# Kernel optimization log

Hardware: AMD Instinct MI355X
Metric: run time of the kernel (lower is better)

Reference implementation:

```python
import jax, jax.numpy as jnp
import numpy as np

ROI_SIZE = 7
MAX_BIN_H = 8   # max adaptive-maxpool bin height for crop H <= 37
MAX_BIN_W = 9   # max adaptive-maxpool bin width  for crop W <= 50
SCALE = 0.0625  # 1/16 feature stride


def setup_inputs() -> dict:
    key = jax.random.key(0)
    ks = jax.random.split(key, 12)
    B, C, h, w = 1, 512, 37, 50          # conv5 feature map of a 600x800 image
    N = 512                               # number of ROIs (proposals)
    n_class = 21
    d_in, d_fc = C * ROI_SIZE * ROI_SIZE, 4096
    x = jax.random.normal(ks[0], (B, C, h, w), dtype=jnp.float32)
    # rois in image coordinates (x1, y1, x2, y2), image is 800x600
    x1 = jax.random.uniform(ks[1], (N,), minval=0.0, maxval=700.0)
    y1 = jax.random.uniform(ks[2], (N,), minval=0.0, maxval=500.0)
    bw = jax.random.uniform(ks[3], (N,), minval=16.0, maxval=400.0)
    bh = jax.random.uniform(ks[4], (N,), minval=16.0, maxval=300.0)
    rois = jnp.stack([x1, y1, jnp.minimum(x1 + bw, 799.0), jnp.minimum(y1 + bh, 599.0)], axis=1).astype(jnp.float32)
    roi_index = jnp.zeros((N,), dtype=jnp.int32)  # single image in batch
    W1 = jax.random.normal(ks[5], (d_in, d_fc), dtype=jnp.float32) * 0.01
    b1 = jnp.zeros((d_fc,), dtype=jnp.float32)
    W2 = jax.random.normal(ks[6], (d_fc, d_fc), dtype=jnp.float32) * 0.01
    b2 = jnp.zeros((d_fc,), dtype=jnp.float32)
    Wp = jax.random.normal(ks[7], (d_fc, n_class * 4), dtype=jnp.float32) * 0.001
    bp = jax.random.normal(ks[8], (n_class * 4,), dtype=jnp.float32) * 0.001
    Ws = jax.random.normal(ks[9], (d_fc, n_class), dtype=jnp.float32) * 0.01
    bs = jax.random.normal(ks[10], (n_class,), dtype=jnp.float32) * 0.01
    return dict(x=x, rois=rois, roi_index=roi_index, W1=W1, b1=b1, W2=W2, b2=b2, Wp=Wp, bp=bp, Ws=Ws, bs=bs)


def _roi_pool(x, rois, roi_index):
    """Faithful port of roi_pooling(): per-ROI crop + AdaptiveMaxPool2d(7)."""
    B, C, h, w = x.shape
    S = ROI_SIZE
    coords = jnp.round(rois * SCALE)  # round-half-even, like torch.round
    cx1 = jnp.clip(coords[:, 0], 0, w).astype(jnp.int32)
    cy1 = jnp.clip(coords[:, 1], 0, h).astype(jnp.int32)
    cx2 = jnp.clip(coords[:, 2], 0, w).astype(jnp.int32)
    cy2 = jnp.clip(coords[:, 3], 0, h).astype(jnp.int32)
    bidx = roi_index.astype(jnp.int32)
    roi_stack = jnp.stack([bidx, cx1, cy1, cx2, cy2], axis=1)  # [N,5]

    def pool_one(carry, roi):
        bi, x1i, y1i, x2i, y2i = roi[0], roi[1], roi[2], roi[3], roi[4]
        valid = (x1i < x2i) & (y1i < y2i)
        # torch slicing roi[2]:roi[4]+1 silently truncates at the tensor edge
        x2e = jnp.minimum(x2i, w - 1)
        y2e = jnp.minimum(y2i, h - 1)
        Hc = y2e - y1i + 1
        Wc = x2e - x1i + 1
        i = jnp.arange(S)
        # adaptive max pool bins: [floor(i*H/S), ceil((i+1)*H/S))
        rs = y1i + (i * Hc) // S
        re = y1i + ((i + 1) * Hc + S - 1) // S
        cs = x1i + (i * Wc) // S
        ce = x1i + ((i + 1) * Wc + S - 1) // S
        rows = rs[:, None] + jnp.arange(MAX_BIN_H)          # [S, MBH]
        rmask = rows < re[:, None]
        rows = jnp.clip(rows, 0, h - 1)
        cols = cs[:, None] + jnp.arange(MAX_BIN_W)          # [S, MBW]
        cmask = cols < ce[:, None]
        cols = jnp.clip(cols, 0, w - 1)
        feat = x[bi]                                         # [C, h, w]
        g = feat[:, rows[:, None, :, None], cols[None, :, None, :]]  # [C,S,S,MBH,MBW]
        mask = rmask[:, None, :, None] & cmask[None, :, None, :]     # [S,S,MBH,MBW]
        pooled = jnp.where(mask, g, -jnp.inf).max(axis=(-2, -1))    # [C,S,S]
        pooled = jnp.where(valid, pooled, jnp.zeros_like(pooled))
        return carry, pooled

    _, out = jax.lax.scan(pool_one, None, roi_stack)  # [N, C, S, S]
    return out


def reference(x, rois, roi_index, W1, b1, W2, b2, Wp, bp, Ws, bs):
    pooled = _roi_pool(x, rois, roi_index)            # [N, 512, 7, 7]
    flat = pooled.reshape(pooled.shape[0], -1)        # [N, 25088]
    fc6 = jax.nn.relu(flat @ W1 + b1)                 # [N, 4096]
    fc7 = jax.nn.relu(fc6 @ W2 + b2)                  # [N, 4096]
    roi_class_params = fc7 @ Wp + bp                  # [N, n_class*4]
    roi_scores = fc7 @ Ws + bs                        # [N, n_class]
    return (roi_class_params, roi_scores)
```

## Files before the change

kernel.cpp:

```cpp
#include <hip/hip_runtime.h>
#include <hip/hip_bf16.h>

using f32x4  = float          __attribute__((ext_vector_type(4)));
using bf16x8 = __bf16         __attribute__((ext_vector_type(8)));
using u16x8  = unsigned short __attribute__((ext_vector_type(8)));

#define C_CH 512
#define H_IN 37
#define W_IN 50
#define NPOS 1850
#define NROI 512
#define DIN  25088
#define DFC  4096
#define NPAR 84
#define NCLS 21
#define KS1  4
#define KS2  4
#define KSH  8

#define PB_X  232
#define PB_WH 2048
#define PB_TOT (PB_X + PB_WH)

__device__ __forceinline__ unsigned pack_bf16x2(float a, float b) {
    __hip_bfloat162 h;
    h.x = __float2bfloat16(a);
    h.y = __float2bfloat16(b);
    return *reinterpret_cast<unsigned*>(&h);
}

__device__ __forceinline__ void gload_lds16(const void* src, void* dst) {
    __builtin_amdgcn_global_load_lds(
        (const __attribute__((address_space(1))) void*)src,
        (__attribute__((address_space(3))) void*)dst, 16, 0, 0);
}

__global__ __launch_bounds__(256) void prep_kernel(
        const float* __restrict__ x, float* __restrict__ xt,
        const float* __restrict__ Wp, const float* __restrict__ Ws,
        float* __restrict__ Whp) {
    __shared__ float tile[64][65];
    int b = blockIdx.x;
    int t = threadIdx.x;
    if (b < PB_X) {
        int p0 = (b % 29) * 64;
        int c0 = (b / 29) * 64;
        int tc = t & 63, tr = t >> 6;
#pragma unroll
        for (int i = 0; i < 16; ++i) {
            int r = tr + i * 4;
            int p = p0 + tc;
            float v = 0.f;
            if (p < NPOS) v = x[(size_t)(c0 + r) * NPOS + p];
            tile[r][tc] = v;
        }
        __syncthreads();
#pragma unroll
        for (int i = 0; i < 16; ++i) {
            int rw = tr + i * 4;
            int p = p0 + rw;
            if (p < NPOS) xt[(size_t)p * C_CH + c0 + tc] = tile[tc][rw];
        }
    } else {
        int idx = (b - PB_X) * 256 + t;
        int k = idx >> 7, c = idx & 127;
        float v = 0.f;
        if (c < NPAR) v = Wp[(size_t)k * NPAR + c];
        else if (c < NPAR + NCLS) v = Ws[(size_t)k * NCLS + (c - NPAR)];
        Whp[idx] = v;
    }
}

__global__ __launch_bounds__(256) void roi_pool_kernel(
        const float* __restrict__ xt, const float* __restrict__ rois,
        __hip_bfloat16* __restrict__ pooled) {
    int n = blockIdx.x;
    int t = threadIdx.x;
    float4 rv = reinterpret_cast<const float4*>(rois)[n];
    int x1 = (int)fminf(fmaxf(rintf(rv.x * 0.0625f), 0.f), (float)W_IN);
    int y1 = (int)fminf(fmaxf(rintf(rv.y * 0.0625f), 0.f), (float)H_IN);
    int x2 = (int)fminf(fmaxf(rintf(rv.z * 0.0625f), 0.f), (float)W_IN);
    int y2 = (int)fminf(fmaxf(rintf(rv.w * 0.0625f), 0.f), (float)H_IN);
    bool valid = (x1 < x2) && (y1 < y2);
    unsigned* outp = reinterpret_cast<unsigned*>(pooled) + (size_t)n * (DIN / 2);
    if (!valid) {
        for (int b = 0; b < 49; ++b) outp[b * 256 + t] = 0u;
        return;
    }
    int x2e = min(x2, W_IN - 1), y2e = min(y2, H_IN - 1);
    int Hc = y2e - y1 + 1, Wc = x2e - x1 + 1;
    const float2* base = reinterpret_cast<const float2*>(xt);
    for (int i = 0; i < 7; ++i) {
        int rs = y1 + (i * Hc) / 7;
        int re = y1 + ((i + 1) * Hc + 6) / 7;
        for (int j = 0; j < 7; ++j) {
            int cs = x1 + (j * Wc) / 7;
            int ce = x1 + ((j + 1) * Wc + 6) / 7;
            float m0 = -__builtin_inff(), m1 = -__builtin_inff();
            for (int r = rs; r < re; ++r) {
                const float2* rowp = base + (size_t)r * (W_IN * C_CH / 2) + t;
                for (int c = cs; c < ce; ++c) {
                    float2 v = rowp[c * (C_CH / 2)];
                    m0 = fmaxf(m0, v.x);
                    m1 = fmaxf(m1, v.y);
                }
            }
            outp[(i * 7 + j) * 256 + t] = pack_bf16x2(m0, m1);
        }
    }
}

__global__ __launch_bounds__(256) void gemm_f32b_kernel(
        const __hip_bfloat16* __restrict__ A,
        const float* __restrict__ Bf,
        float* __restrict__ Cp,
        int N, int lda, int ldbn, int kChunk, int nMT, int nNT, int Mtot,
        int perm) {
    __shared__ __align__(16) char lA[3 * 16384];
    __shared__ __align__(16) char lB[2 * 16384];

    int q = gridDim.x >> 3;
    int bid = (blockIdx.x & 7) * q + (blockIdx.x >> 3);
    int mt = bid % nMT;
    int nt = (bid / nMT) % nNT;
    int ks = bid / (nMT * nNT);
    int m0 = mt * 128, n0 = nt * 128;
    int k0 = ks * kChunk;
    int t = threadIdx.x;
    int lane = t & 63, wid = t >> 6;

    const char* srcA[4]; int offA[4];
#pragma unroll
    for (int i = 0; i < 4; ++i) {
        int chunk = i * 4 + wid;
        int p = chunk * 1024 + lane * 16;
        int row = p >> 7;
        int swz = ((row ^ (row >> 3)) & 7) << 4;
        srcA[i] = (const char*)A + ((size_t)(m0 + row) * lda + k0) * 2
                  + ((p & 127) ^ swz);
        offA[i] = chunk * 1024;
    }
    auto stageA = [&](char* slot) {
#pragma unroll
        for (int i = 0; i < 4; ++i) {
            gload_lds16(srcA[i], slot + offA[i]);
            srcA[i] += 128;
        }
    };

    int n4 = (t & 31) * 4;
    int k8 = (t >> 5) * 8;
    int rstr = perm ? 49 : 1;
    const float* pB = Bf + n0 + n4;
    int koff[8];
#pragma unroll
    for (int p = 0; p < 8; ++p) koff[p] = (k8 + p) * rstr * ldbn;
    int woff[4];
#pragma unroll
    for (int j = 0; j < 4; ++j) {
        int row = n4 + j;
        int swz = ((row ^ (row >> 3)) & 7) << 4;
        woff[j] = row * 128 + ((k8 * 2) ^ swz);
    }
    auto loadB = [&](int kt, f32x4 (&v)[8]) {
        int kb = k0 + (kt << 6);
        int rb = perm ? ((kb & 511) * 49 + (kb >> 9)) : kb;
        int rbo = rb * ldbn;
#pragma unroll
        for (int p = 0; p < 8; ++p)
            v[p] = *reinterpret_cast<const f32x4*>(pB + (size_t)(rbo + koff[p]));
    };
    auto cvtB = [&](f32x4 (&v)[8], char* bW) {
#pragma unroll
        for (int j = 0; j < 4; ++j) {
            uint4 w;
            w.x = pack_bf16x2(v[0][j], v[1][j]);
            w.y = pack_bf16x2(v[2][j], v[3][j]);
            w.z = pack_bf16x2(v[4][j], v[5][j]);
            w.w = pack_bf16x2(v[6][j], v[7][j]);
            *reinterpret_cast<uint4*>(bW + woff[j]) = w;
        }
    };

    int wm = wid >> 1, wn = wid & 1;
    int kb0 = (lane >> 4) << 4;
    int roA[4], roB[4], sA[4], sB[4];
#pragma unroll
    for (int f = 0; f < 4; ++f) {
        int ra = wm * 64 + f * 16 + (lane & 15);
        int rb = wn * 64 + f * 16 + (lane & 15);
        roA[f] = ra * 128; sA[f] = ((ra ^ (ra >> 3)) & 7) << 4;
        roB[f] = rb * 128; sB[f] = ((rb ^ (rb >> 3)) & 7) << 4;
    }

    f32x4 acc[4][4] = {};
    auto mfmaHalf = [&](const char* bA, const char* bB, int ksub) {
        int kk = kb0 | (ksub << 6);
        bf16x8 af[4], bfr[4];
#pragma unroll
        for (int f = 0; f < 4; ++f)
            af[f] = *reinterpret_cast<const bf16x8*>(bA + roA[f] + (kk ^ sA[f]));
#pragma unroll
        for (int f = 0; f < 4; ++f)
            bfr[f] = *reinterpret_cast<const bf16x8*>(bB + roB[f] + (kk ^ sB[f]));
#pragma unroll
        for (int mf = 0; mf < 4; ++mf)
#pragma unroll
            for (int nf = 0; nf < 4; ++nf)
                acc[mf][nf] = __builtin_amdgcn_mfma_f32_16x16x32_bf16(
                    af[mf], bfr[nf], acc[mf][nf], 0, 0, 0);
    };

    int nkt = kChunk >> 6;

    f32x4 vP[8], vQ[8];
    auto body = [&](int tt, char* aR, char* aS,
                    f32x4 (&vC)[8], char* bR, char* bW) {
        mfmaHalf(aR, bR, 0);
        if (tt + 1 < nkt) cvtB(vC, bW);
        mfmaHalf(aR, bR, 1);
        if (tt + 2 < nkt) stageA(aS);
        if (tt + 3 < nkt) {
            loadB(tt + 3, vC);
            asm volatile("s_waitcnt vmcnt(12) lgkmcnt(0)\ns_barrier" ::: "memory");
        } else {
            asm volatile("s_waitcnt vmcnt(0) lgkmcnt(0)\ns_barrier" ::: "memory");
        }
    };

    stageA(lA);
    stageA(lA + 16384);
    loadB(0, vP);
    loadB(1, vQ);
    cvtB(vP, lB);
    loadB(2, vP);
    asm volatile("s_waitcnt vmcnt(12) lgkmcnt(0)\ns_barrier" ::: "memory");

    char* s0 = lA;  char* s1 = lA + 16384;  char* s2 = lA + 32768;
    char* b0 = lB;  char* b1 = lB + 16384;
    for (int kt = 0; kt < nkt; kt += 6) {
        body(kt + 0, s0, s2, vQ, b0, b1);
        if (kt + 1 < nkt) body(kt + 1, s1, s0, vP, b1, b0);
        if (kt + 2 < nkt) body(kt + 2, s2, s1, vQ, b0, b1);
        if (kt + 3 < nkt) body(kt + 3, s0, s2, vP, b1, b0);
        if (kt + 4 < nkt) body(kt + 4, s1, s0, vQ, b0, b1);
        if (kt + 5 < nkt) body(kt + 5, s2, s1, vP, b1, b0);
    }

    float* outp = Cp + (size_t)ks * Mtot * N;
    int rbase = m0 + wm * 64;
    int cbase = n0 + wn * 64 + (lane & 15);
    int rl = (lane >> 4) * 4;
#pragma unroll
    for (int mf = 0; mf < 4; ++mf)
#pragma unroll
        for (int nf = 0; nf < 4; ++nf)
#pragma unroll
            for (int r = 0; r < 4; ++r)
                outp[(size_t)(rbase + mf * 16 + rl + r) * N + cbase + nf * 16] =
                    acc[mf][nf][r];
}

__global__ __launch_bounds__(256) void reduce_bias_relu_kernel(
        const float* __restrict__ P, const float* __restrict__ bias,
        __hip_bfloat16* __restrict__ out, int MN, int N, int KS) {
    int idx = blockIdx.x * blockDim.x + threadIdx.x;
    int e0 = idx * 4;
    if (e0 >= MN) return;
    f32x4 s = *reinterpret_cast<const f32x4*>(P + e0);
    for (int k = 1; k < KS; ++k)
        s += *reinterpret_cast<const f32x4*>(P + (size_t)k * MN + e0);
    f32x4 b = *reinterpret_cast<const f32x4*>(bias + (e0 & (N - 1)));
    s += b;
    uint2 pk;
    pk.x = pack_bf16x2(fmaxf(s[0], 0.f), fmaxf(s[1], 0.f));
    pk.y = pack_bf16x2(fmaxf(s[2], 0.f), fmaxf(s[3], 0.f));
    *reinterpret_cast<uint2*>(reinterpret_cast<char*>(out) + (size_t)e0 * 2) = pk;
}

__global__ __launch_bounds__(128) void head_reduce_kernel(
        const float* __restrict__ P, const float* __restrict__ bp,
        const float* __restrict__ bs, float* __restrict__ out, int KS) {
    int n = blockIdx.x, c = threadIdx.x;
    float s = 0.f;
    for (int ks = 0; ks < KS; ++ks)
        s += P[(size_t)ks * NROI * 128 + (size_t)n * 128 + c];
    if (c < NPAR)
        out[(size_t)n * NPAR + c] = s + bp[c];
    else if (c < NPAR + NCLS)
        out[(size_t)NROI * NPAR + (size_t)n * NCLS + (c - NPAR)] = s + bs[c - NPAR];
}

extern "C" void kernel_launch(void* const* d_in, const int* in_sizes, int n_in,
                              void* d_out, int out_size, void* d_ws, size_t ws_size,
                              hipStream_t stream) {
    const float* x    = (const float*)d_in[0];
    const float* rois = (const float*)d_in[1];
    const float* W1 = (const float*)d_in[3];
    const float* b1 = (const float*)d_in[4];
    const float* W2 = (const float*)d_in[5];
    const float* b2 = (const float*)d_in[6];
    const float* Wp = (const float*)d_in[7];
    const float* bp = (const float*)d_in[8];
    const float* Ws = (const float*)d_in[9];
    const float* bs = (const float*)d_in[10];
    float* out = (float*)d_out;

    const size_t MB = 1ull << 20;
    char* ws = (char*)d_ws;
    float*          xt     = (float*)(ws + 0);
    __hip_bfloat16* pooled = (__hip_bfloat16*)(ws + 4   * MB);
    float*          Whp    = (float*)(ws + 30  * MB);
    float*          part   = (float*)(ws + 34  * MB);
    __hip_bfloat16* fc6    = (__hip_bfloat16*)(ws + 104 * MB);
    __hip_bfloat16* fc7    = (__hip_bfloat16*)(ws + 109 * MB);

    prep_kernel<<<PB_TOT, 256, 0, stream>>>(x, xt, Wp, Ws, Whp);
    roi_pool_kernel<<<NROI, 256, 0, stream>>>(xt, rois, pooled);

    gemm_f32b_kernel<<<4 * 32 * KS1, 256, 0, stream>>>(
        pooled, W1, part, DFC, DIN, DFC, DIN / KS1, 4, 32, NROI, 1);
    reduce_bias_relu_kernel<<<2048, 256, 0, stream>>>(part, b1, fc6,
                                                      NROI * DFC, DFC, KS1);

    gemm_f32b_kernel<<<4 * 32 * KS2, 256, 0, stream>>>(
        fc6, W2, part, DFC, DFC, DFC, DFC / KS2, 4, 32, NROI, 0);
    reduce_bias_relu_kernel<<<2048, 256, 0, stream>>>(part, b2, fc7,
                                                      NROI * DFC, DFC, KS2);

    gemm_f32b_kernel<<<4 * KSH, 256, 0, stream>>>(fc7, Whp, part,
                                                  128, DFC, 128, DFC / KSH,
                                                  4, 1, NROI, 0);
    head_reduce_kernel<<<NROI, 128, 0, stream>>>(part, bp, bs, out, KSH);
}
```

Before: 391.8 us.

## Shrink GEMM LDS ring and double split-K to raise occupancy

```diff
diff --git a/kernel.cpp b/kernel.cpp
--- a/kernel.cpp
+++ b/kernel.cpp
@@ -14,9 +14,9 @@
 #define DFC  4096
 #define NPAR 84
 #define NCLS 21
-#define KS1  4
-#define KS2  4
-#define KSH  8
+#define KS1  8
+#define KS2  8
+#define KSH  16
 
 #define PB_X  232
 #define PB_WH 2048
@@ -110,14 +110,15 @@
     }
 }
 
-__global__ __launch_bounds__(256) void gemm_f32b_kernel(
+__global__ __launch_bounds__(256, 3) void gemm_f32b_kernel(
         const __hip_bfloat16* __restrict__ A,
         const float* __restrict__ Bf,
         float* __restrict__ Cp,
         int N, int lda, int ldbn, int kChunk, int nMT, int nNT, int Mtot,
         int perm) {
-    __shared__ __align__(16) char lA[3 * 16384];
-    __shared__ __align__(16) char lB[2 * 16384];
+    __shared__ __align__(16) char lA0[16384];
+    __shared__ __align__(16) char lA1[16384];
+    __shared__ __align__(16) char lB[16384];
 
     int q = gridDim.x >> 3;
     int bid = (blockIdx.x & 7) * q + (blockIdx.x >> 3);
@@ -162,7 +163,8 @@
         int swz = ((row ^ (row >> 3)) & 7) << 4;
         woff[j] = row * 128 + ((k8 * 2) ^ swz);
     }
-    auto loadB = [&](int kt, f32x4 (&v)[8]) {
+    f32x4 v[8];
+    auto loadB = [&](int kt) {
         int kb = k0 + (kt << 6);
         int rb = perm ? ((kb & 511) * 49 + (kb >> 9)) : kb;
         int rbo = rb * ldbn;
@@ -170,7 +172,7 @@
         for (int p = 0; p < 8; ++p)
             v[p] = *reinterpret_cast<const f32x4*>(pB + (size_t)(rbo + koff[p]));
     };
-    auto cvtB = [&](f32x4 (&v)[8], char* bW) {
+    auto cvtB = [&]() {
 #pragma unroll
         for (int j = 0; j < 4; ++j) {
             uint4 w;
@@ -178,7 +180,7 @@
             w.y = pack_bf16x2(v[2][j], v[3][j]);
             w.z = pack_bf16x2(v[4][j], v[5][j]);
             w.w = pack_bf16x2(v[6][j], v[7][j]);
-            *reinterpret_cast<uint4*>(bW + woff[j]) = w;
+            *reinterpret_cast<uint4*>(lB + woff[j]) = w;
         }
     };
 
@@ -194,58 +196,49 @@
     }
 
     f32x4 acc[4][4] = {};
-    auto mfmaHalf = [&](const char* bA, const char* bB, int ksub) {
-        int kk = kb0 | (ksub << 6);
-        bf16x8 af[4], bfr[4];
-#pragma unroll
-        for (int f = 0; f < 4; ++f)
-            af[f] = *reinterpret_cast<const bf16x8*>(bA + roA[f] + (kk ^ sA[f]));
-#pragma unroll
-        for (int f = 0; f < 4; ++f)
-            bfr[f] = *reinterpret_cast<const bf16x8*>(bB + roB[f] + (kk ^ sB[f]));
-#pragma unroll
-        for (int mf = 0; mf < 4; ++mf)
-#pragma unroll
-            for (int nf = 0; nf < 4; ++nf)
-                acc[mf][nf] = __builtin_amdgcn_mfma_f32_16x16x32_bf16(
-                    af[mf], bfr[nf], acc[mf][nf], 0, 0, 0);
+    auto mfmaTile = [&](const char* bA) {
+#pragma unroll
+        for (int ksub = 0; ksub < 2; ++ksub) {
+            int kk = kb0 | (ksub << 6);
+            bf16x8 af[4], bfr[4];
+#pragma unroll
+            for (int f = 0; f < 4; ++f)
+                af[f] = *reinterpret_cast<const bf16x8*>(bA + roA[f] + (kk ^ sA[f]));
+#pragma unroll
+            for (int f = 0; f < 4; ++f)
+                bfr[f] = *reinterpret_cast<const bf16x8*>(lB + roB[f] + (kk ^ sB[f]));
+#pragma unroll
+            for (int mf = 0; mf < 4; ++mf)
+#pragma unroll
+                for (int nf = 0; nf < 4; ++nf)
+                    acc[mf][nf] = __builtin_amdgcn_mfma_f32_16x16x32_bf16(
+                        af[mf], bfr[nf], acc[mf][nf], 0, 0, 0);
+        }
     };
 
     int nkt = kChunk >> 6;
 
-    f32x4 vP[8], vQ[8];
-    auto body = [&](int tt, char* aR, char* aS,
-                    f32x4 (&vC)[8], char* bR, char* bW) {
-        mfmaHalf(aR, bR, 0);
-        if (tt + 1 < nkt) cvtB(vC, bW);
-        mfmaHalf(aR, bR, 1);
-        if (tt + 2 < nkt) stageA(aS);
-        if (tt + 3 < nkt) {
-            loadB(tt + 3, vC);
-            asm volatile("s_waitcnt vmcnt(12) lgkmcnt(0)\ns_barrier" ::: "memory");
+    auto body = [&](int tt, const char* curA, char* nxtA) {
+        cvtB();
+        if (tt + 1 < nkt) {
+            loadB(tt + 1);
+            stageA(nxtA);
+            asm volatile("s_waitcnt vmcnt(12) lgkmcnt(0)" ::: "memory");
         } else {
-            asm volatile("s_waitcnt vmcnt(0) lgkmcnt(0)\ns_barrier" ::: "memory");
-        }
-    };
-
-    stageA(lA);
-    stageA(lA + 16384);
-    loadB(0, vP);
-    loadB(1, vQ);
-    cvtB(vP, lB);
-    loadB(2, vP);
-    asm volatile("s_waitcnt vmcnt(12) lgkmcnt(0)\ns_barrier" ::: "memory");
-
-    char* s0 = lA;  char* s1 = lA + 16384;  char* s2 = lA + 32768;
-    char* b0 = lB;  char* b1 = lB + 16384;
-    for (int kt = 0; kt < nkt; kt += 6) {
-        body(kt + 0, s0, s2, vQ, b0, b1);
-        if (kt + 1 < nkt) body(kt + 1, s1, s0, vP, b1, b0);
-        if (kt + 2 < nkt) body(kt + 2, s2, s1, vQ, b0, b1);
-        if (kt + 3 < nkt) body(kt + 3, s0, s2, vP, b1, b0);
-        if (kt + 4 < nkt) body(kt + 4, s1, s0, vQ, b0, b1);
-        if (kt + 5 < nkt) body(kt + 5, s2, s1, vP, b1, b0);
-    }
+            asm volatile("s_waitcnt vmcnt(0) lgkmcnt(0)" ::: "memory");
+        }
+        __builtin_amdgcn_s_barrier();
+        mfmaTile(curA);
+        __builtin_amdgcn_s_barrier();
+    };
+
+    loadB(0);
+    stageA(lA0);
+    for (int kt = 0; kt + 1 < nkt; kt += 2) {
+        body(kt, lA0, lA1);
+        body(kt + 1, lA1, lA0);
+    }
+    if (nkt & 1) body(nkt - 1, lA0, lA1);
 
     float* outp = Cp + (size_t)ks * Mtot * N;
     int rbase = m0 + wm * 64;
```

Measured after the change: 826.3 us. +110.9%, slower.
